# Performance work log

Measured on AMD Instinct MI355X. Metric: run time of the kernel, lower is better.

The kernel has to match this reference:

```python
import jax, jax.numpy as jnp
import numpy as np

L = 2      # layer_num
H = 64     # hid_dim == in_dim (required by final .view(B, N, F))


def setup_inputs() -> dict:
    key = jax.random.key(0)
    k = jax.random.split(key, 5)
    B, T, N, Fd = 64, 48, 256, H
    s = 1.0 / np.sqrt(H)  # PyTorch GRUCell init scale
    return {
        "x": jax.random.normal(k[0], (B, T, N, Fd), dtype=jnp.float32),
        "Wih": jax.random.uniform(k[1], (L, 3 * H, H), minval=-s, maxval=s, dtype=jnp.float32),
        "Whh": jax.random.uniform(k[2], (L, 3 * H, H), minval=-s, maxval=s, dtype=jnp.float32),
        "bih": jax.random.uniform(k[3], (L, 3 * H), minval=-s, maxval=s, dtype=jnp.float32),
        "bhh": jax.random.uniform(k[4], (L, 3 * H), minval=-s, maxval=s, dtype=jnp.float32),
    }


def _ngru_forward(x, Wih, Whh, bih, bhh):
    B, T, N, Fd = x.shape
    # (T, B*N, F): time-major sequence; each layer sees the SAME input x_t
    # (layers are parallel, not stacked, per the original module).
    xs = x.transpose(1, 0, 2, 3).reshape(T, B * N, Fd)
    h0 = jnp.zeros((L, B * N, H), dtype=x.dtype)

    def step(h, x_t):
        # gi: (L, B*N, 3H), gh: (L, B*N, 3H)
        gi = jnp.einsum('bf,lgf->lbg', x_t, Wih) + bih[:, None, :]
        gh = jnp.einsum('lbh,lgh->lbg', h, Whh) + bhh[:, None, :]
        gi_r, gi_z, gi_n = jnp.split(gi, 3, axis=-1)
        gh_r, gh_z, gh_n = jnp.split(gh, 3, axis=-1)
        r = jax.nn.sigmoid(gi_r + gh_r)
        z = jax.nn.sigmoid(gi_z + gh_z)
        n = jnp.tanh(gi_n + r * gh_n)
        h_new = (1.0 - z) * n + z * h
        return h_new, None

    h_final, _ = jax.lax.scan(step, h0, xs)
    # out = h of LAST layer, viewed back as (B, N, F) (requires H == Fd)
    return h_final[-1].reshape(B, N, H)


def reference(x, Wih, Whh, bih, bhh):
    return _ngru_forward(x, Wih, Whh, bih, bhh)
```

## Files before the change

### kernel.cpp

```cpp
#include <hip/hip_runtime.h>
#include <math.h>


#define TT 48
#define HH 64
#define GG 192
#define NN 256
#define RPB 32
#define NTHREADS 256
#define AK 136
#define HBUF (RPB*AK)

typedef _Float16 h8 __attribute__((ext_vector_type(8)));
typedef __attribute__((ext_vector_type(4))) float f32x4;
typedef __attribute__((ext_vector_type(4))) unsigned u32x4;

__device__ __forceinline__ float sigm(float v) {
    return __builtin_amdgcn_rcpf(1.f + __expf(-v));
}
__device__ __forceinline__ float tanh_f(float v) {
    float a = fabsf(v);
    float e = __expf(2.f * a);
    float t = 1.f - 2.f * __builtin_amdgcn_rcpf(e + 1.f);
    return v < 0.f ? -t : t;
}
__device__ __forceinline__ unsigned pkh2(float a, float b) {
    union { _Float16 h[2]; unsigned u; } c;
    c.h[0] = (_Float16)a; c.h[1] = (_Float16)b;
    return c.u;
}

__global__ __launch_bounds__(NTHREADS)
__attribute__((amdgpu_waves_per_eu(2, 2)))
void ngru_mfma9(const float* __restrict__ x,
                const float* __restrict__ Wih,
                const float* __restrict__ Whh,
                const float* __restrict__ bih,
                const float* __restrict__ bhh,
                float* __restrict__ out)
{
    extern __shared__ __align__(16) _Float16 lds_h[];

    const int tid  = threadIdx.x;
    const int lane = tid & 63;
    const int nw   = tid >> 6;
    const int c0   = lane & 15;
    const int rq   = lane >> 4;
    const int j    = nw * 16 + c0;

    const int grow0 = blockIdx.x * RPB;
    const int bb    = grow0 / NN;
    const int n0    = grow0 % NN;

    const float* Wi = Wih + GG * HH;
    const float* Wh = Whh + GG * HH;

    h8 Bf[12];
    #pragma unroll
    for (int g = 0; g < 4; ++g) {
        const int ktlo = (g == 3) ? 2 : 0;
        const int kthi = (g == 2) ? 2 : 4;
        #pragma unroll
        for (int kt = ktlo; kt < kthi; ++kt) {
            const int slot = (g < 2) ? g * 4 + kt : 8 + (g - 2) * 2 + (kt & 1);
            const bool isWi = (kt < 2);
            const int gbase = (g >= 2) ? 2 : g;
            const float* src = (isWi ? Wi : Wh)
                             + (gbase * 64 + j) * HH + (kt & 1) * 32 + rq * 8;
            h8 f;
            #pragma unroll
            for (int q = 0; q < 8; ++q) f[q] = (_Float16)src[q];
            Bf[slot] = f;
        }
    }

    const float brz  = bih[GG + j]      + bhh[GG + j];
    const float bzz  = bih[GG + 64 + j] + bhh[GG + 64 + j];
    const float bi_n = bih[GG + 128 + j];
    const float bh_n = bhh[GG + 128 + j];

    const int xrow = tid >> 3;
    const int xkc  = (tid & 7) * 8;
    {
        *(u32x4*)(lds_h + xrow * AK + 64 + xkc) = (u32x4){0u, 0u, 0u, 0u};

        const float* xsrc = x + ((size_t)(bb * TT) * NN + n0 + xrow) * HH + xkc;
        float4 p0 = *(const float4*)xsrc;
        float4 p1 = *(const float4*)(xsrc + 4);
        u32x4 w = {pkh2(p0.x, p0.y), pkh2(p0.z, p0.w),
                   pkh2(p1.x, p1.y), pkh2(p1.z, p1.w)};
        *(u32x4*)(lds_h + xrow * AK + xkc) = w;
    }

    float hreg[2][4];
    #pragma unroll
    for (int m = 0; m < 2; ++m)
        #pragma unroll
        for (int r = 0; r < 4; ++r) hreg[m][r] = 0.f;

    __syncthreads();

    for (int t = 0; t < TT; ++t) {
        _Float16* cur = lds_h + (t & 1) * HBUF;
        _Float16* nxt = lds_h + ((t & 1) ^ 1) * HBUF;
        const bool hasNext = (t + 1 < TT);

        float4 p0, p1;
        if (hasNext) {
            const float* xsrc =
                x + ((size_t)(bb * TT + t + 1) * NN + n0 + xrow) * HH + xkc;
            p0 = *(const float4*)xsrc;
            p1 = *(const float4*)(xsrc + 4);
        }

        f32x4 acc[2][4];
        #pragma unroll
        for (int m = 0; m < 2; ++m) {
            acc[m][0] = (f32x4){brz,  brz,  brz,  brz };
            acc[m][1] = (f32x4){bzz,  bzz,  bzz,  bzz };
            acc[m][2] = (f32x4){bi_n, bi_n, bi_n, bi_n};
            acc[m][3] = (f32x4){bh_n, bh_n, bh_n, bh_n};
        }

        __builtin_amdgcn_s_setprio(1);
        #pragma unroll
        for (int m = 0; m < 2; ++m) {
            const _Float16* ab = cur + (m * 16 + c0) * AK + rq * 8;
            h8 A_[4];
            #pragma unroll
            for (int kt = 0; kt < 4; ++kt)
                A_[kt] = *(const h8*)(ab + kt * 32);
            #pragma unroll
            for (int g = 0; g < 4; ++g) {
                #pragma unroll
                for (int kt = 0; kt < 4; ++kt) {
                    if ((g == 2 && kt >= 2) || (g == 3 && kt < 2)) continue;
                    const int slot = (g < 2) ? g * 4 + kt
                                             : 8 + (g - 2) * 2 + (kt & 1);
                    acc[m][g] = __builtin_amdgcn_mfma_f32_16x16x32_f16(
                        A_[kt], Bf[slot], acc[m][g], 0, 0, 0);
                }
            }
        }
        __builtin_amdgcn_s_setprio(0);

        #pragma unroll
        for (int m = 0; m < 2; ++m) {
            #pragma unroll
            for (int r = 0; r < 4; ++r) {
                const int row = m * 16 + rq * 4 + r;
                float rg = sigm(acc[m][0][r]);
                float zg = sigm(acc[m][1][r]);
                float ng = tanh_f(fmaf(rg, acc[m][3][r], acc[m][2][r]));
                float hn = fmaf(zg, hreg[m][r] - ng, ng);
                hreg[m][r] = hn;
                if (hasNext)
                    nxt[row * AK + 64 + j] = (_Float16)hn;
            }
        }

        if (hasNext) {
            u32x4 w = {pkh2(p0.x, p0.y), pkh2(p0.z, p0.w),
                       pkh2(p1.x, p1.y), pkh2(p1.z, p1.w)};
            *(u32x4*)(nxt + xrow * AK + xkc) = w;
            __syncthreads();
        }
    }

    #pragma unroll
    for (int m = 0; m < 2; ++m)
        #pragma unroll
        for (int r = 0; r < 4; ++r)
            out[(size_t)(grow0 + m * 16 + rq * 4 + r) * HH + j] = hreg[m][r];
}

extern "C" void kernel_launch(void* const* d_in, const int* in_sizes, int n_in,
                              void* d_out, int out_size, void* d_ws, size_t ws_size,
                              hipStream_t stream) {
    const float* x   = (const float*)d_in[0];
    const float* Wih = (const float*)d_in[1];
    const float* Whh = (const float*)d_in[2];
    const float* bih = (const float*)d_in[3];
    const float* bhh = (const float*)d_in[4];
    float* out = (float*)d_out;

    const int lds_bytes = 2 * HBUF * (int)sizeof(_Float16);
    (void)hipFuncSetAttribute((const void*)ngru_mfma9,
                        hipFuncAttributeMaxDynamicSharedMemorySize, lds_bytes);

    dim3 grid(16384 / RPB);
    dim3 block(NTHREADS);
    ngru_mfma9<<<grid, block, lds_bytes, stream>>>(x, Wih, Whh, bih, bhh, out);
}
```

Baseline: 67.90 us.

## Precompute next-step input projection in registers, removing x from LDS

```diff
diff --git a/kernel.cpp b/kernel.cpp
--- a/kernel.cpp
+++ b/kernel.cpp
@@ -8,8 +8,8 @@
 #define NN 256
 #define RPB 32
 #define NTHREADS 256
-#define AK 136
-#define HBUF (RPB*AK)
+#define HK 72
+#define HBUF (RPB*HK)
 
 typedef _Float16 h8 __attribute__((ext_vector_type(8)));
 typedef __attribute__((ext_vector_type(4))) float f32x4;
@@ -29,15 +29,22 @@
     c.h[0] = (_Float16)a; c.h[1] = (_Float16)b;
     return c.u;
 }
+__device__ __forceinline__ h8 cvt_frag(float4 a, float4 b) {
+    u32x4 w = {pkh2(a.x, a.y), pkh2(a.z, a.w),
+               pkh2(b.x, b.y), pkh2(b.z, b.w)};
+    return __builtin_bit_cast(h8, w);
+}
+
+#define MF(A, B, C) __builtin_amdgcn_mfma_f32_16x16x32_f16(A, B, C, 0, 0, 0)
 
 __global__ __launch_bounds__(NTHREADS)
 __attribute__((amdgpu_waves_per_eu(2, 2)))
-void ngru_mfma9(const float* __restrict__ x,
-                const float* __restrict__ Wih,
-                const float* __restrict__ Whh,
-                const float* __restrict__ bih,
-                const float* __restrict__ bhh,
-                float* __restrict__ out)
+void ngru_mfma10(const float* __restrict__ x,
+                 const float* __restrict__ Wih,
+                 const float* __restrict__ Whh,
+                 const float* __restrict__ bih,
+                 const float* __restrict__ bhh,
+                 float* __restrict__ out)
 {
     extern __shared__ __align__(16) _Float16 lds_h[];
 
@@ -57,39 +64,54 @@
 
     h8 Bf[12];
     #pragma unroll
-    for (int g = 0; g < 4; ++g) {
-        const int ktlo = (g == 3) ? 2 : 0;
-        const int kthi = (g == 2) ? 2 : 4;
-        #pragma unroll
-        for (int kt = ktlo; kt < kthi; ++kt) {
-            const int slot = (g < 2) ? g * 4 + kt : 8 + (g - 2) * 2 + (kt & 1);
-            const bool isWi = (kt < 2);
-            const int gbase = (g >= 2) ? 2 : g;
-            const float* src = (isWi ? Wi : Wh)
-                             + (gbase * 64 + j) * HH + (kt & 1) * 32 + rq * 8;
-            h8 f;
+    for (int g = 0; g < 3; ++g) {
+        #pragma unroll
+        for (int kt = 0; kt < 2; ++kt) {
+            const float* si = Wi + (g * 64 + j) * HH + kt * 32 + rq * 8;
+            const float* sh = Wh + (g * 64 + j) * HH + kt * 32 + rq * 8;
+            h8 fi, fh;
             #pragma unroll
-            for (int q = 0; q < 8; ++q) f[q] = (_Float16)src[q];
-            Bf[slot] = f;
+            for (int q = 0; q < 8; ++q) {
+                fi[q] = (_Float16)si[q];
+                fh[q] = (_Float16)sh[q];
+            }
+            Bf[g * 2 + kt]     = fi;
+            Bf[6 + g * 2 + kt] = fh;
         }
     }
 
     const float brz  = bih[GG + j]      + bhh[GG + j];
     const float bzz  = bih[GG + 64 + j] + bhh[GG + 64 + j];
-    const float bi_n = bih[GG + 128 + j];
-    const float bh_n = bhh[GG + 128 + j];
-
-    const int xrow = tid >> 3;
-    const int xkc  = (tid & 7) * 8;
+    const float bin_ = bih[GG + 128 + j];
+    const float bhn_ = bhh[GG + 128 + j];
+    const f32x4 BIASr = {brz,  brz,  brz,  brz };
+    const f32x4 BIASz = {bzz,  bzz,  bzz,  bzz };
+    const f32x4 BIASi = {bin_, bin_, bin_, bin_};
+    const f32x4 BIASh = {bhn_, bhn_, bhn_, bhn_};
+
+    for (int idx = tid; idx < HBUF / 8; idx += NTHREADS)
+        *(u32x4*)(lds_h + idx * 8) = (u32x4){0u, 0u, 0u, 0u};
+
+    f32x4 accA[2][4], accB[2][4];
     {
-        *(u32x4*)(lds_h + xrow * AK + 64 + xkc) = (u32x4){0u, 0u, 0u, 0u};
-
-        const float* xsrc = x + ((size_t)(bb * TT) * NN + n0 + xrow) * HH + xkc;
-        float4 p0 = *(const float4*)xsrc;
-        float4 p1 = *(const float4*)(xsrc + 4);
-        u32x4 w = {pkh2(p0.x, p0.y), pkh2(p0.z, p0.w),
-                   pkh2(p1.x, p1.y), pkh2(p1.z, p1.w)};
-        *(u32x4*)(lds_h + xrow * AK + xkc) = w;
+        const float* xb = x + ((size_t)(bb * TT) * NN + n0) * HH;
+        h8 Xf[2][2];
+        #pragma unroll
+        for (int m = 0; m < 2; ++m)
+            #pragma unroll
+            for (int kt = 0; kt < 2; ++kt) {
+                const float* s_ = xb + (m * 16 + c0) * HH + kt * 32 + rq * 8;
+                Xf[m][kt] = cvt_frag(*(const float4*)s_, *(const float4*)(s_ + 4));
+            }
+        #pragma unroll
+        for (int m = 0; m < 2; ++m) {
+            accA[m][0] = MF(Xf[m][0], Bf[0], BIASr);
+            accA[m][0] = MF(Xf[m][1], Bf[1], accA[m][0]);
+            accA[m][1] = MF(Xf[m][0], Bf[2], BIASz);
+            accA[m][1] = MF(Xf[m][1], Bf[3], accA[m][1]);
+            accA[m][2] = MF(Xf[m][0], Bf[4], BIASi);
+            accA[m][2] = MF(Xf[m][1], Bf[5], accA[m][2]);
+        }
     }
 
     float hreg[2][4];
@@ -100,72 +122,78 @@
 
     __syncthreads();
 
-    for (int t = 0; t < TT; ++t) {
-        _Float16* cur = lds_h + (t & 1) * HBUF;
-        _Float16* nxt = lds_h + ((t & 1) ^ 1) * HBUF;
-        const bool hasNext = (t + 1 < TT);
-
-        float4 p0, p1;
-        if (hasNext) {
-            const float* xsrc =
-                x + ((size_t)(bb * TT + t + 1) * NN + n0 + xrow) * HH + xkc;
-            p0 = *(const float4*)xsrc;
-            p1 = *(const float4*)(xsrc + 4);
-        }
-
-        f32x4 acc[2][4];
-        #pragma unroll
-        for (int m = 0; m < 2; ++m) {
-            acc[m][0] = (f32x4){brz,  brz,  brz,  brz };
-            acc[m][1] = (f32x4){bzz,  bzz,  bzz,  bzz };
-            acc[m][2] = (f32x4){bi_n, bi_n, bi_n, bi_n};
-            acc[m][3] = (f32x4){bh_n, bh_n, bh_n, bh_n};
-        }
-
-        __builtin_amdgcn_s_setprio(1);
-        #pragma unroll
-        for (int m = 0; m < 2; ++m) {
-            const _Float16* ab = cur + (m * 16 + c0) * AK + rq * 8;
-            h8 A_[4];
-            #pragma unroll
-            for (int kt = 0; kt < 4; ++kt)
-                A_[kt] = *(const h8*)(ab + kt * 32);
-            #pragma unroll
-            for (int g = 0; g < 4; ++g) {
-                #pragma unroll
-                for (int kt = 0; kt < 4; ++kt) {
-                    if ((g == 2 && kt >= 2) || (g == 3 && kt < 2)) continue;
-                    const int slot = (g < 2) ? g * 4 + kt
-                                             : 8 + (g - 2) * 2 + (kt & 1);
-                    acc[m][g] = __builtin_amdgcn_mfma_f32_16x16x32_f16(
-                        A_[kt], Bf[slot], acc[m][g], 0, 0, 0);
-                }
-            }
-        }
-        __builtin_amdgcn_s_setprio(0);
-
-        #pragma unroll
-        for (int m = 0; m < 2; ++m) {
-            #pragma unroll
-            for (int r = 0; r < 4; ++r) {
-                const int row = m * 16 + rq * 4 + r;
-                float rg = sigm(acc[m][0][r]);
-                float zg = sigm(acc[m][1][r]);
-                float ng = tanh_f(fmaf(rg, acc[m][3][r], acc[m][2][r]));
-                float hn = fmaf(zg, hreg[m][r] - ng, ng);
-                hreg[m][r] = hn;
-                if (hasNext)
-                    nxt[row * AK + 64 + j] = (_Float16)hn;
-            }
-        }
-
-        if (hasNext) {
-            u32x4 w = {pkh2(p0.x, p0.y), pkh2(p0.z, p0.w),
-                       pkh2(p1.x, p1.y), pkh2(p1.z, p1.w)};
-            *(u32x4*)(nxt + xrow * AK + xkc) = w;
-            __syncthreads();
-        }
-    }
+#define BODY(ACCC, ACCN, T)                                                    \
+    {                                                                          \
+        const int t_ = (T);                                                    \
+        _Float16* cur = lds_h + (t_ & 1) * HBUF;                               \
+        _Float16* nxt = lds_h + ((t_ & 1) ^ 1) * HBUF;                         \
+        const bool hasNext = (t_ + 1 < TT);                                    \
+                         \
+        h8 Hf[2][2];                                                           \
+        _Pragma("unroll") for (int m = 0; m < 2; ++m)                          \
+            _Pragma("unroll") for (int kt = 0; kt < 2; ++kt)                   \
+                Hf[m][kt] = *(const h8*)(cur + (m*16 + c0)*HK + kt*32 + rq*8); \
+               \
+        float4 pa[2][2], pb[2][2];                                             \
+        if (hasNext) {                                                         \
+            const float* xb = x + ((size_t)(bb*TT + t_ + 1)*NN + n0)*HH;       \
+            _Pragma("unroll") for (int m = 0; m < 2; ++m)                      \
+                _Pragma("unroll") for (int kt = 0; kt < 2; ++kt) {             \
+                    const float* s_ = xb + (m*16 + c0)*HH + kt*32 + rq*8;      \
+                    pa[m][kt] = *(const float4*)s_;                            \
+                    pb[m][kt] = *(const float4*)(s_ + 4);                      \
+                }                                                              \
+        }                                                                      \
+                                        \
+        __builtin_amdgcn_s_setprio(1);                                         \
+        _Pragma("unroll") for (int m = 0; m < 2; ++m) {                        \
+            ACCC[m][0] = MF(Hf[m][0], Bf[6],  ACCC[m][0]);                     \
+            ACCC[m][0] = MF(Hf[m][1], Bf[7],  ACCC[m][0]);                     \
+            ACCC[m][1] = MF(Hf[m][0], Bf[8],  ACCC[m][1]);                     \
+            ACCC[m][1] = MF(Hf[m][1], Bf[9],  ACCC[m][1]);                     \
+            ACCC[m][3] = MF(Hf[m][0], Bf[10], BIASh);                          \
+            ACCC[m][3] = MF(Hf[m][1], Bf[11], ACCC[m][3]);                     \
+        }                                                                      \
+        __builtin_amdgcn_s_setprio(0);                                         \
+                          \
+        _Pragma("unroll") for (int m = 0; m < 2; ++m) {                        \
+            _Pragma("unroll") for (int r = 0; r < 4; ++r) {                    \
+                const int row = m * 16 + rq * 4 + r;                           \
+                float rg = sigm(ACCC[m][0][r]);                                \
+                float zg = sigm(ACCC[m][1][r]);                                \
+                float ng = tanh_f(fmaf(rg, ACCC[m][3][r], ACCC[m][2][r]));     \
+                float hn = fmaf(zg, hreg[m][r] - ng, ng);                      \
+                hreg[m][r] = hn;                                               \
+                if (hasNext)                                                   \
+                    nxt[row * HK + j] = (_Float16)hn;        \
+            }                                                                  \
+        }                                                                      \
+        if (hasNext) {                                                         \
+               \
+            h8 Xf[2][2];                                                       \
+            _Pragma("unroll") for (int m = 0; m < 2; ++m)                      \
+                _Pragma("unroll") for (int kt = 0; kt < 2; ++kt)               \
+                    Xf[m][kt] = cvt_frag(pa[m][kt], pb[m][kt]);                \
+                  \
+            __builtin_amdgcn_s_setprio(1);                                     \
+            _Pragma("unroll") for (int m = 0; m < 2; ++m) {                    \
+                ACCN[m][0] = MF(Xf[m][0], Bf[0], BIASr);                       \
+                ACCN[m][0] = MF(Xf[m][1], Bf[1], ACCN[m][0]);                  \
+                ACCN[m][1] = MF(Xf[m][0], Bf[2], BIASz);                       \
+                ACCN[m][1] = MF(Xf[m][1], Bf[3], ACCN[m][1]);                  \
+                ACCN[m][2] = MF(Xf[m][0], Bf[4], BIASi);                       \
+                ACCN[m][2] = MF(Xf[m][1], Bf[5], ACCN[m][2]);                  \
+            }                                                                  \
+            __builtin_amdgcn_s_setprio(0);                                     \
+            __syncthreads();              \
+        }                                                                      \
+    }
+
+    for (int tt = 0; tt < TT; tt += 2) {
+        BODY(accA, accB, tt);
+        BODY(accB, accA, tt + 1);
+    }
+#undef BODY
 
     #pragma unroll
     for (int m = 0; m < 2; ++m)
@@ -185,10 +213,10 @@
     float* out = (float*)d_out;
 
     const int lds_bytes = 2 * HBUF * (int)sizeof(_Float16);
-    (void)hipFuncSetAttribute((const void*)ngru_mfma9,
+    (void)hipFuncSetAttribute((const void*)ngru_mfma10,
                         hipFuncAttributeMaxDynamicSharedMemorySize, lds_bytes);
 
     dim3 grid(16384 / RPB);
     dim3 block(NTHREADS);
-    ngru_mfma9<<<grid, block, lds_bytes, stream>>>(x, Wih, Whh, bih, bhh, out);
-}
+    ngru_mfma10<<<grid, block, lds_bytes, stream>>>(x, Wih, Whh, bih, bhh, out);
+}
```

Result: slower. 118.2 us (+74.1%).

## Keep x fragments in registers and double rows per block with 8 waves

Applied to the files above, without the earlier changes.

```diff
diff --git a/kernel.cpp b/kernel.cpp
--- a/kernel.cpp
+++ b/kernel.cpp
@@ -6,10 +6,10 @@
 #define HH 64
 #define GG 192
 #define NN 256
-#define RPB 32
-#define NTHREADS 256
-#define AK 136
-#define HBUF (RPB*AK)
+#define RPB 64
+#define NTHREADS 512
+#define HK 72
+#define HBUF (RPB*HK)
 
 typedef _Float16 h8 __attribute__((ext_vector_type(8)));
 typedef __attribute__((ext_vector_type(4))) float f32x4;
@@ -29,24 +29,34 @@
     c.h[0] = (_Float16)a; c.h[1] = (_Float16)b;
     return c.u;
 }
+__device__ __forceinline__ h8 cvt_frag(float4 a, float4 b) {
+    u32x4 w = {pkh2(a.x, a.y), pkh2(a.z, a.w),
+               pkh2(b.x, b.y), pkh2(b.z, b.w)};
+    return __builtin_bit_cast(h8, w);
+}
+
+#define MF(A, B, C) __builtin_amdgcn_mfma_f32_16x16x32_f16(A, B, C, 0, 0, 0)
 
 __global__ __launch_bounds__(NTHREADS)
 __attribute__((amdgpu_waves_per_eu(2, 2)))
-void ngru_mfma9(const float* __restrict__ x,
-                const float* __restrict__ Wih,
-                const float* __restrict__ Whh,
-                const float* __restrict__ bih,
-                const float* __restrict__ bhh,
-                float* __restrict__ out)
+void ngru_mfma14(const float* __restrict__ x,
+                 const float* __restrict__ Wih,
+                 const float* __restrict__ Whh,
+                 const float* __restrict__ bih,
+                 const float* __restrict__ bhh,
+                 float* __restrict__ out)
 {
     extern __shared__ __align__(16) _Float16 lds_h[];
 
     const int tid  = threadIdx.x;
     const int lane = tid & 63;
-    const int nw   = tid >> 6;
+    const int wv   = tid >> 6;
+    const int mq   = wv >> 2;
+    const int nw   = wv & 3;
     const int c0   = lane & 15;
     const int rq   = lane >> 4;
     const int j    = nw * 16 + c0;
+    const int rbase = mq * 32;
 
     const int grow0 = blockIdx.x * RPB;
     const int bb    = grow0 / NN;
@@ -76,20 +86,24 @@
 
     const float brz  = bih[GG + j]      + bhh[GG + j];
     const float bzz  = bih[GG + 64 + j] + bhh[GG + 64 + j];
-    const float bi_n = bih[GG + 128 + j];
-    const float bh_n = bhh[GG + 128 + j];
-
-    const int xrow = tid >> 3;
-    const int xkc  = (tid & 7) * 8;
+    const float bin_ = bih[GG + 128 + j];
+    const float bhn_ = bhh[GG + 128 + j];
+
+    for (int idx = tid; idx < HBUF / 2; idx += NTHREADS)
+        *(unsigned*)(lds_h + idx * 2) = 0u;
+
+    h8 Xf[2][2];
     {
-        *(u32x4*)(lds_h + xrow * AK + 64 + xkc) = (u32x4){0u, 0u, 0u, 0u};
-
-        const float* xsrc = x + ((size_t)(bb * TT) * NN + n0 + xrow) * HH + xkc;
-        float4 p0 = *(const float4*)xsrc;
-        float4 p1 = *(const float4*)(xsrc + 4);
-        u32x4 w = {pkh2(p0.x, p0.y), pkh2(p0.z, p0.w),
-                   pkh2(p1.x, p1.y), pkh2(p1.z, p1.w)};
-        *(u32x4*)(lds_h + xrow * AK + xkc) = w;
+        const float* xb = x + ((size_t)(bb * TT) * NN + n0) * HH;
+        #pragma unroll
+        for (int m = 0; m < 2; ++m)
+            #pragma unroll
+            for (int kt = 0; kt < 2; ++kt) {
+                const float* s_ = xb + (rbase + m * 16 + c0) * HH
+                                + kt * 32 + rq * 8;
+                Xf[m][kt] = cvt_frag(*(const float4*)s_,
+                                     *(const float4*)(s_ + 4));
+            }
     }
 
     float hreg[2][4];
@@ -105,64 +119,74 @@
         _Float16* nxt = lds_h + ((t & 1) ^ 1) * HBUF;
         const bool hasNext = (t + 1 < TT);
 
-        float4 p0, p1;
+        float4 pa[2][2], pb[2][2];
         if (hasNext) {
-            const float* xsrc =
-                x + ((size_t)(bb * TT + t + 1) * NN + n0 + xrow) * HH + xkc;
-            p0 = *(const float4*)xsrc;
-            p1 = *(const float4*)(xsrc + 4);
-        }
-
-        f32x4 acc[2][4];
-        #pragma unroll
-        for (int m = 0; m < 2; ++m) {
-            acc[m][0] = (f32x4){brz,  brz,  brz,  brz };
-            acc[m][1] = (f32x4){bzz,  bzz,  bzz,  bzz };
-            acc[m][2] = (f32x4){bi_n, bi_n, bi_n, bi_n};
-            acc[m][3] = (f32x4){bh_n, bh_n, bh_n, bh_n};
-        }
+            const float* xb = x + ((size_t)(bb * TT + t + 1) * NN + n0) * HH;
+            #pragma unroll
+            for (int m = 0; m < 2; ++m)
+                #pragma unroll
+                for (int kt = 0; kt < 2; ++kt) {
+                    const float* s_ = xb + (rbase + m * 16 + c0) * HH
+                                    + kt * 32 + rq * 8;
+                    pa[m][kt] = *(const float4*)s_;
+                    pb[m][kt] = *(const float4*)(s_ + 4);
+                }
+        }
+
+        h8 Hf[2][2];
+        #pragma unroll
+        for (int m = 0; m < 2; ++m)
+            #pragma unroll
+            for (int kt = 0; kt < 2; ++kt)
+                Hf[m][kt] = *(const h8*)(cur + (rbase + m * 16 + c0) * HK
+                                         + kt * 32 + rq * 8);
+
+        f32x4 a00 = {brz,  brz,  brz,  brz };
+        f32x4 a01 = {bzz,  bzz,  bzz,  bzz };
+        f32x4 a02 = {bin_, bin_, bin_, bin_};
+        f32x4 a03 = {bhn_, bhn_, bhn_, bhn_};
+        f32x4 a10 = a00, a11 = a01, a12 = a02, a13 = a03;
 
         __builtin_amdgcn_s_setprio(1);
-        #pragma unroll
-        for (int m = 0; m < 2; ++m) {
-            const _Float16* ab = cur + (m * 16 + c0) * AK + rq * 8;
-            h8 A_[4];
-            #pragma unroll
-            for (int kt = 0; kt < 4; ++kt)
-                A_[kt] = *(const h8*)(ab + kt * 32);
-            #pragma unroll
-            for (int g = 0; g < 4; ++g) {
+        a00 = MF(Xf[0][0], Bf[0], a00);  a00 = MF(Xf[0][1], Bf[1], a00);
+        a10 = MF(Xf[1][0], Bf[0], a10);  a10 = MF(Xf[1][1], Bf[1], a10);
+        a01 = MF(Xf[0][0], Bf[4], a01);  a01 = MF(Xf[0][1], Bf[5], a01);
+        a11 = MF(Xf[1][0], Bf[4], a11);  a11 = MF(Xf[1][1], Bf[5], a11);
+        a02 = MF(Xf[0][0], Bf[8], a02);  a02 = MF(Xf[0][1], Bf[9], a02);
+        a12 = MF(Xf[1][0], Bf[8], a12);  a12 = MF(Xf[1][1], Bf[9], a12);
+        a00 = MF(Hf[0][0], Bf[2], a00);  a00 = MF(Hf[0][1], Bf[3], a00);
+        a10 = MF(Hf[1][0], Bf[2], a10);  a10 = MF(Hf[1][1], Bf[3], a10);
+        a01 = MF(Hf[0][0], Bf[6], a01);  a01 = MF(Hf[0][1], Bf[7], a01);
+        a11 = MF(Hf[1][0], Bf[6], a11);  a11 = MF(Hf[1][1], Bf[7], a11);
+        a03 = MF(Hf[0][0], Bf[10], a03); a03 = MF(Hf[0][1], Bf[11], a03);
+        a13 = MF(Hf[1][0], Bf[10], a13); a13 = MF(Hf[1][1], Bf[11], a13);
+        __builtin_amdgcn_s_setprio(0);
+
+        #pragma unroll
+        for (int r = 0; r < 4; ++r) {
+            const int row0 = rbase + rq * 4 + r;
+            float rg0 = sigm(a00[r]);
+            float zg0 = sigm(a01[r]);
+            float ng0 = tanh_f(fmaf(rg0, a03[r], a02[r]));
+            float hn0 = fmaf(zg0, hreg[0][r] - ng0, ng0);
+            hreg[0][r] = hn0;
+            float rg1 = sigm(a10[r]);
+            float zg1 = sigm(a11[r]);
+            float ng1 = tanh_f(fmaf(rg1, a13[r], a12[r]));
+            float hn1 = fmaf(zg1, hreg[1][r] - ng1, ng1);
+            hreg[1][r] = hn1;
+            if (hasNext) {
+                nxt[row0 * HK + j]        = (_Float16)hn0;
+                nxt[(row0 + 16) * HK + j] = (_Float16)hn1;
+            }
+        }
+
+        if (hasNext) {
+            #pragma unroll
+            for (int m = 0; m < 2; ++m)
                 #pragma unroll
-                for (int kt = 0; kt < 4; ++kt) {
-                    if ((g == 2 && kt >= 2) || (g == 3 && kt < 2)) continue;
-                    const int slot = (g < 2) ? g * 4 + kt
-                                             : 8 + (g - 2) * 2 + (kt & 1);
-                    acc[m][g] = __builtin_amdgcn_mfma_f32_16x16x32_f16(
-                        A_[kt], Bf[slot], acc[m][g], 0, 0, 0);
-                }
-            }
-        }
-        __builtin_amdgcn_s_setprio(0);
-
-        #pragma unroll
-        for (int m = 0; m < 2; ++m) {
-            #pragma unroll
-            for (int r = 0; r < 4; ++r) {
-                const int row = m * 16 + rq * 4 + r;
-                float rg = sigm(acc[m][0][r]);
-                float zg = sigm(acc[m][1][r]);
-                float ng = tanh_f(fmaf(rg, acc[m][3][r], acc[m][2][r]));
-                float hn = fmaf(zg, hreg[m][r] - ng, ng);
-                hreg[m][r] = hn;
-                if (hasNext)
-                    nxt[row * AK + 64 + j] = (_Float16)hn;
-            }
-        }
-
-        if (hasNext) {
-            u32x4 w = {pkh2(p0.x, p0.y), pkh2(p0.z, p0.w),
-                       pkh2(p1.x, p1.y), pkh2(p1.z, p1.w)};
-            *(u32x4*)(nxt + xrow * AK + xkc) = w;
+                for (int kt = 0; kt < 2; ++kt)
+                    Xf[m][kt] = cvt_frag(pa[m][kt], pb[m][kt]);
             __syncthreads();
         }
     }
@@ -171,7 +195,8 @@
     for (int m = 0; m < 2; ++m)
         #pragma unroll
         for (int r = 0; r < 4; ++r)
-            out[(size_t)(grow0 + m * 16 + rq * 4 + r) * HH + j] = hreg[m][r];
+            out[(size_t)(grow0 + rbase + m * 16 + rq * 4 + r) * HH + j] =
+                hreg[m][r];
 }
 
 extern "C" void kernel_launch(void* const* d_in, const int* in_sizes, int n_in,
@@ -185,10 +210,10 @@
     float* out = (float*)d_out;
 
     const int lds_bytes = 2 * HBUF * (int)sizeof(_Float16);
-    (void)hipFuncSetAttribute((const void*)ngru_mfma9,
+    (void)hipFuncSetAttribute((const void*)ngru_mfma14,
                         hipFuncAttributeMaxDynamicSharedMemorySize, lds_bytes);
 
     dim3 grid(16384 / RPB);
     dim3 block(NTHREADS);
-    ngru_mfma9<<<grid, block, lds_bytes, stream>>>(x, Wih, Whh, bih, bhh, out);
-}
+    ngru_mfma14<<<grid, block, lds_bytes, stream>>>(x, Wih, Whh, bih, bhh, out);
+}
```

Measured after the change: 123.6 us. +82.0%, slower.
